# Performance work log

Hardware: AMD Instinct MI355X
Metric: run time of the kernel (lower is better)

The kernel has to match this reference:

```python
import jax, jax.numpy as jnp
import numpy as np

B, M, ND, ED, D, H = 4, 1024, 64, 8, 64, 4
ALPHA = 0.2
NEG = -9.0e15


def setup_inputs() -> dict:
    key = jax.random.key(0)
    ks = jax.random.split(key, 6)
    h = jax.random.normal(ks[0], (B, M, ND), jnp.float32)
    mch_mask = jax.random.randint(ks[1], (B, M, M), 0, 2).astype(jnp.int32)
    comp_val = jax.random.normal(ks[2], (B, M, M, ED), jnp.float32)
    W = jax.random.normal(ks[3], (H, ND, D), jnp.float32) * 0.1
    W_edge = jax.random.normal(ks[4], (H, ED, D), jnp.float32) * 0.1
    a = jax.random.normal(ks[5], (H, 3 * D), jnp.float32) * 0.1
    return {"h": h, "mch_mask": mch_mask, "comp_val": comp_val,
            "W": W, "W_edge": W_edge, "a": a}


def reference(h, mch_mask, comp_val, W, W_edge, a):
    # h: [B,M,ND], mch_mask: [B,M,M], comp_val: [B,M,M,ED]
    # W: [H,ND,D], W_edge: [H,ED,D], a: [H,3D]  (heads stacked)
    d = W.shape[-1]
    a1, a2, a3 = a[:, :d], a[:, d:2 * d], a[:, 2 * d:]
    Wh = jnp.einsum('bmd,hde->bhme', h, W)              # [B,H,M,D]
    Wh1 = jnp.einsum('bhme,he->bhm', Wh, a1)            # [B,H,M]
    Wh2 = jnp.einsum('bhme,he->bhm', Wh, a2)            # [B,H,M]
    # edge_feas = (comp_val @ W_edge) @ a3, fused: comp_val @ (W_edge @ a3)
    w_e = jnp.einsum('hed,hd->he', W_edge, a3)          # [H,ED]
    edge_feas = jnp.einsum('bkqe,he->bhkq', comp_val, w_e)  # [B,H,M,M]
    e = Wh1[:, :, :, None] + Wh2[:, :, None, :] + edge_feas
    e = jnp.where(e > 0, e, ALPHA * e)                  # leaky_relu
    e = jnp.where(mch_mask[:, None, :, :] > 0, e, NEG)
    attn = jax.nn.softmax(e, axis=-1)                   # [B,H,M,M]
    h_prime = jnp.einsum('bhkq,bhqd->bhkd', attn, Wh)   # [B,H,M,D]
    b, nh, m, dd = h_prime.shape
    return h_prime.transpose(0, 2, 1, 3).reshape(b, m, nh * dd)  # concat heads
```

## Files before the change

kernel.cpp:

```cpp
#include <hip/hip_runtime.h>
#include <hip/hip_bf16.h>

#define B_ 4
#define M_ 1024
#define ND_ 64
#define ED_ 8
#define D_ 64
#define H_ 4
#define KT 16
#define QC 64
#define NCH (M_ / QC)
#define ALPHA 0.2f

#define WS_WH1 1048576
#define WS_WH2 1064960
#define WS_WE  1081344

__device__ __forceinline__ float4 f4fma(float s, const float4& v, float4 a) {
    a.x = fmaf(s, v.x, a.x);
    a.y = fmaf(s, v.y, a.y);
    a.z = fmaf(s, v.z, a.z);
    a.w = fmaf(s, v.w, a.w);
    return a;
}

__global__ __launch_bounds__(256) void k_pre(const float* __restrict__ hg,
                                             const float* __restrict__ Wg,
                                             const float* __restrict__ ag,
                                             float* __restrict__ Whg,
                                             float* __restrict__ Wh1g,
                                             float* __restrict__ Wh2g) {
    const int t = threadIdx.x;
    const int g = blockIdx.x * 256 + t;
    const int d = t & 63;
    const int bhm = g >> 6;
    const int m = bhm & (M_ - 1);
    const int h = (bhm >> 10) & (H_ - 1);
    const int b = bhm >> 12;
    const float* hrow = hg + (b * M_ + m) * ND_;
    const float* wcol = Wg + h * ND_ * D_ + d;
    float acc = 0.f;
#pragma unroll
    for (int i = 0; i < ND_; ++i) acc = fmaf(hrow[i], wcol[i * D_], acc);
    Whg[g] = acc;
    float r1 = acc * ag[h * 192 + d];
    float r2 = acc * ag[h * 192 + 64 + d];
#pragma unroll
    for (int off = 32; off >= 1; off >>= 1) {
        r1 += __shfl_xor(r1, off);
        r2 += __shfl_xor(r2, off);
    }
    if (d == 0) {
        Wh1g[(b * H_ + h) * M_ + m] = r1;
        Wh2g[(b * H_ + h) * M_ + m] = r2;
    }
}

__global__ void k_we(const float* __restrict__ Weg, const float* __restrict__ ag,
                     float* __restrict__ weg) {
    const int t = threadIdx.x;
    if (t < H_ * ED_) {
        const int h = t >> 3, e = t & 7;
        const float* wrow = Weg + (h * ED_ + e) * D_;
        const float* a3 = ag + h * 192 + 128;
        float acc = 0.f;
#pragma unroll
        for (int i = 0; i < D_; ++i) acc = fmaf(wrow[i], a3[i], acc);
        weg[t] = acc;
    }
}

__global__ __launch_bounds__(1024) void k_main(const float* __restrict__ cvg,
                                               const int* __restrict__ mg,
                                               const float* __restrict__ Whg,
                                               const float* __restrict__ Wh1g,
                                               const float* __restrict__ Wh2g,
                                               const float* __restrict__ weg,
                                               float* __restrict__ outg) {
    extern __shared__ float smem[];
    float* whl = smem;
    float* pb = smem + 16384;
    float* wel = smem + 20512;
    float* sl = smem + 20544;
    float4* wh4 = (float4*)whl;
    float4* pb4 = (float4*)pb;
    const float4* we4 = (const float4*)wel;

    const int t = threadIdx.x;
    const int lane = t & 63, wv = t >> 6;
    const int b = blockIdx.x >> 6;
    const int k0 = (blockIdx.x & 63) << 4;
    const int hh = lane >> 4, d4 = lane & 15;

    if (t < 32) wel[t] = weg[t];

    const int ek = k0 + wv;
    float wh1r[H_];
#pragma unroll
    for (int h = 0; h < H_; ++h) wh1r[h] = Wh1g[(b * H_ + h) * M_ + ek];

    float4 acc[4];
#pragma unroll
    for (int i = 0; i < 4; ++i) acc[i] = make_float4(0.f, 0.f, 0.f, 0.f);
    float sreg[H_] = {0.f, 0.f, 0.f, 0.f};

    const float4* cvrow = (const float4*)(cvg + (size_t)(b * M_ + ek) * M_ * ED_);
    const int* mrow = mg + (size_t)(b * M_ + ek) * M_;

#pragma unroll
    for (int i = 0; i < 4; ++i) {
        const int ql = wv * 4 + i;
        const float* src = Whg + ((size_t)((b * H_ + hh) * M_) + ql) * D_ + d4 * 4;
        __builtin_amdgcn_global_load_lds((const __attribute__((address_space(1))) void*)src,
                                         (__attribute__((address_space(3))) void*)(whl + ql * 256),
                                         16, 0, 0);
    }
    float4 cv0 = cvrow[lane * 2 + 0];
    float4 cv1 = cvrow[lane * 2 + 1];
    int mk = mrow[lane];
    float wh2r[H_];
#pragma unroll
    for (int h = 0; h < H_; ++h) wh2r[h] = Wh2g[(b * H_ + h) * M_ + lane];

    __syncthreads();

    for (int c = 0; c < NCH; ++c) {
        float pv[H_];
#pragma unroll
        for (int h = 0; h < H_; ++h) {
            const float4 wa = we4[h * 2], wb = we4[h * 2 + 1];
            float ef = cv0.x * wa.x + cv0.y * wa.y + cv0.z * wa.z + cv0.w * wa.w +
                       cv1.x * wb.x + cv1.y * wb.y + cv1.z * wb.z + cv1.w * wb.w;
            float e = wh1r[h] + wh2r[h] + ef;
            e = fmaxf(e, ALPHA * e);
            pv[h] = (mk > 0) ? __expf(e) : 0.0f;
            pb[h * 1032 + wv * QC + lane] = pv[h];
        }
#pragma unroll
        for (int h = 0; h < H_; ++h) {
            float r = pv[h];
#pragma unroll
            for (int off = 32; off >= 1; off >>= 1) r += __shfl_xor(r, off);
            sreg[h] += r;
        }
        __syncthreads();

        if (c + 1 < NCH) {
            const int qn = (c + 1) * QC + lane;
            cv0 = cvrow[qn * 2 + 0];
            cv1 = cvrow[qn * 2 + 1];
            mk = mrow[qn];
#pragma unroll
            for (int h = 0; h < H_; ++h) wh2r[h] = Wh2g[(b * H_ + h) * M_ + qn];
        }

        {
            const int kq = wv >> 2, qg = wv & 3;
#pragma unroll
            for (int j = 0; j < 4; ++j) {
                const int ql = qg * 16 + j * 4;
                const float4 w0 = wh4[(ql + 0) * 64 + lane];
                const float4 w1 = wh4[(ql + 1) * 64 + lane];
                const float4 w2 = wh4[(ql + 2) * 64 + lane];
                const float4 w3 = wh4[(ql + 3) * 64 + lane];
#pragma unroll
                for (int kk = 0; kk < 4; ++kk) {
                    const float4 pq = pb4[hh * 258 + (kq * 4 + kk) * 16 + (ql >> 2)];
                    float4 a = acc[kk];
                    a = f4fma(pq.x, w0, a);
                    a = f4fma(pq.y, w1, a);
                    a = f4fma(pq.z, w2, a);
                    a = f4fma(pq.w, w3, a);
                    acc[kk] = a;
                }
            }
        }
        __syncthreads();

        if (c + 1 < NCH) {
#pragma unroll
            for (int i = 0; i < 4; ++i) {
                const int ql = wv * 4 + i;
                const float* src =
                    Whg + ((size_t)((b * H_ + hh) * M_) + (c + 1) * QC + ql) * D_ + d4 * 4;
                __builtin_amdgcn_global_load_lds(
                    (const __attribute__((address_space(1))) void*)src,
                    (__attribute__((address_space(3))) void*)(whl + ql * 256), 16, 0, 0);
            }
        }
    }

    if (lane == 0) {
#pragma unroll
        for (int h = 0; h < H_; ++h) sl[wv * H_ + h] = sreg[h];
    }
    __syncthreads();
    {
        const int kq = wv >> 2, qg = wv & 3;
#pragma unroll
        for (int kk = 0; kk < 4; ++kk)
            wh4[((kq * 4 + kk) * 4 + qg) * 64 + lane] = acc[kk];
    }
    __syncthreads();
    {
        const float4 r0 = wh4[(wv * 4 + 0) * 64 + lane];
        const float4 r1 = wh4[(wv * 4 + 1) * 64 + lane];
        const float4 r2 = wh4[(wv * 4 + 2) * 64 + lane];
        const float4 r3 = wh4[(wv * 4 + 3) * 64 + lane];
        const float inv = 1.0f / sl[wv * H_ + hh];
        float4 r;
        r.x = (r0.x + r1.x + r2.x + r3.x) * inv;
        r.y = (r0.y + r1.y + r2.y + r3.y) * inv;
        r.z = (r0.z + r1.z + r2.z + r3.z) * inv;
        r.w = (r0.w + r1.w + r2.w + r3.w) * inv;
        float4* o4 = (float4*)(outg + (size_t)(b * M_ + k0 + wv) * (H_ * D_));
        o4[lane] = r;
    }
}

extern "C" void kernel_launch(void* const* d_in, const int* in_sizes, int n_in,
                              void* d_out, int out_size, void* d_ws, size_t ws_size,
                              hipStream_t stream) {
    const float* hg = (const float*)d_in[0];
    const int* mg = (const int*)d_in[1];
    const float* cvg = (const float*)d_in[2];
    const float* Wg = (const float*)d_in[3];
    const float* Weg = (const float*)d_in[4];
    const float* ag = (const float*)d_in[5];
    float* outg = (float*)d_out;
    float* ws = (float*)d_ws;
    float* Whg = ws;
    float* Wh1g = ws + WS_WH1;
    float* Wh2g = ws + WS_WH2;
    float* weg = ws + WS_WE;

    (void)hipFuncSetAttribute((const void*)k_main,
                              hipFuncAttributeMaxDynamicSharedMemorySize, 82432);

    k_pre<<<4096, 256, 0, stream>>>(hg, Wg, ag, Whg, Wh1g, Wh2g);
    k_we<<<1, 64, 0, stream>>>(Weg, ag, weg);
    k_main<<<256, 1024, 82432, stream>>>(cvg, mg, Whg, Wh1g, Wh2g, weg, outg);
}
```

Measured before the change: 274.3 us.

## Restructure attention kernel to 8-row tiles with per-wave q split and tiled projection

The main kernel now processes 8 query rows per 512-thread block instead of 16 per 1024-thread block, doubling the grid. Each wave owns a slice of the key dimension and keeps 8 row accumulators, with a final cross-wave reduction through LDS. Wh staging switches from async global-to-LDS loads to register-staged prefetch with a padded stride to cut bank conflicts, and the softmax row-sum shuffle reduction moves out of the loop. The projection kernel is also rewritten to stage W and h in LDS and compute four outputs per thread. The trade-offs are more register pressure and Wh being reloaded by twice as many blocks.

Measured after the change: 363.1 us. 32.4% more time.

```diff
diff --git a/kernel.cpp b/kernel.cpp
--- a/kernel.cpp
+++ b/kernel.cpp
@@ -1,5 +1,7 @@
 #include <hip/hip_runtime.h>
 #include <hip/hip_bf16.h>
+
+typedef float v4f __attribute__((ext_vector_type(4)));
 
 #define B_ 4
 #define M_ 1024
@@ -7,7 +9,7 @@
 #define ED_ 8
 #define D_ 64
 #define H_ 4
-#define KT 16
+#define KT 8
 #define QC 64
 #define NCH (M_ / QC)
 #define ALPHA 0.2f
@@ -16,12 +18,25 @@
 #define WS_WH2 1064960
 #define WS_WE  1081344
 
-__device__ __forceinline__ float4 f4fma(float s, const float4& v, float4 a) {
-    a.x = fmaf(s, v.x, a.x);
-    a.y = fmaf(s, v.y, a.y);
-    a.z = fmaf(s, v.z, a.z);
-    a.w = fmaf(s, v.w, a.w);
-    return a;
+#define WHL_STRIDE 260
+#define WHL_F (QC * WHL_STRIDE)
+#define PB_H 520
+#define PB_F (H_ * PB_H)
+#define LDS_BYTES ((WHL_F + PB_F + 32 + 32) * 4)
+
+__device__ __forceinline__ v4f splat(float s) { return (v4f){s, s, s, s}; }
+
+__device__ __forceinline__ v4f f4fma(v4f a, v4f b, v4f c) {
+#if __has_builtin(__builtin_elementwise_fma)
+    return __builtin_elementwise_fma(a, b, c);
+#else
+    v4f r;
+    r.x = fmaf(a.x, b.x, c.x);
+    r.y = fmaf(a.y, b.y, c.y);
+    r.z = fmaf(a.z, b.z, c.z);
+    r.w = fmaf(a.w, b.w, c.w);
+    return r;
+#endif
 }
 
 __global__ __launch_bounds__(256) void k_pre(const float* __restrict__ hg,
@@ -30,29 +45,53 @@
                                              float* __restrict__ Whg,
                                              float* __restrict__ Wh1g,
                                              float* __restrict__ Wh2g) {
-    const int t = threadIdx.x;
-    const int g = blockIdx.x * 256 + t;
-    const int d = t & 63;
-    const int bhm = g >> 6;
-    const int m = bhm & (M_ - 1);
-    const int h = (bhm >> 10) & (H_ - 1);
-    const int b = bhm >> 12;
-    const float* hrow = hg + (b * M_ + m) * ND_;
-    const float* wcol = Wg + h * ND_ * D_ + d;
-    float acc = 0.f;
-#pragma unroll
-    for (int i = 0; i < ND_; ++i) acc = fmaf(hrow[i], wcol[i * D_], acc);
-    Whg[g] = acc;
-    float r1 = acc * ag[h * 192 + d];
-    float r2 = acc * ag[h * 192 + 64 + d];
-#pragma unroll
-    for (int off = 32; off >= 1; off >>= 1) {
+    __shared__ float wl[ND_ * D_];
+    __shared__ float hl[16 * 68];
+    const int t = threadIdx.x, lane = t & 63, wv = t >> 6;
+    const int bid = blockIdx.x;
+    const int b = bid >> 8, h = (bid >> 6) & (H_ - 1), mb = bid & 63;
+    const int m0 = mb * 16;
+
+    {
+        const float* wsrc = Wg + h * ND_ * D_;
+#pragma unroll
+        for (int i = 0; i < 4; ++i) {
+            const float* s = wsrc + (wv * 4 + i) * 256 + lane * 4;
+            __builtin_amdgcn_global_load_lds(
+                (const __attribute__((address_space(1))) void*)s,
+                (__attribute__((address_space(3))) void*)(wl + (wv * 4 + i) * 256), 16, 0, 0);
+        }
+    }
+    {
+        const int mh = t >> 4, u = t & 15;
+        v4f hv = *(const v4f*)(hg + ((size_t)(b * M_) + m0 + mh) * ND_ + u * 4);
+        *(v4f*)(hl + mh * 68 + u * 4) = hv;
+    }
+    __syncthreads();
+
+    const int m = t >> 4, d4 = t & 15;
+    v4f acc = {0.f, 0.f, 0.f, 0.f};
+#pragma unroll
+    for (int i = 0; i < ND_; ++i) {
+        v4f w4 = *(const v4f*)(wl + i * 64 + d4 * 4);
+        float hs = hl[m * 68 + i];
+        acc = f4fma(splat(hs), w4, acc);
+    }
+    *(v4f*)(Whg + (((size_t)(b * H_ + h)) * M_ + m0 + m) * D_ + d4 * 4) = acc;
+
+    v4f a1 = *(const v4f*)(ag + h * 192 + d4 * 4);
+    v4f a2 = *(const v4f*)(ag + h * 192 + 64 + d4 * 4);
+    v4f p1 = acc * a1, p2 = acc * a2;
+    float r1 = (p1.x + p1.y) + (p1.z + p1.w);
+    float r2 = (p2.x + p2.y) + (p2.z + p2.w);
+#pragma unroll
+    for (int off = 8; off >= 1; off >>= 1) {
         r1 += __shfl_xor(r1, off);
         r2 += __shfl_xor(r2, off);
     }
-    if (d == 0) {
-        Wh1g[(b * H_ + h) * M_ + m] = r1;
-        Wh2g[(b * H_ + h) * M_ + m] = r2;
+    if (d4 == 0) {
+        Wh1g[((size_t)(b * H_ + h)) * M_ + m0 + m] = r1;
+        Wh2g[((size_t)(b * H_ + h)) * M_ + m0 + m] = r2;
     }
 }
 
@@ -70,26 +109,22 @@
     }
 }
 
-__global__ __launch_bounds__(1024) void k_main(const float* __restrict__ cvg,
-                                               const int* __restrict__ mg,
-                                               const float* __restrict__ Whg,
-                                               const float* __restrict__ Wh1g,
-                                               const float* __restrict__ Wh2g,
-                                               const float* __restrict__ weg,
-                                               float* __restrict__ outg) {
+__global__ __launch_bounds__(512, 4) void k_main(const float* __restrict__ cvg,
+                                                 const int* __restrict__ mg,
+                                                 const float* __restrict__ Whg,
+                                                 const float* __restrict__ Wh1g,
+                                                 const float* __restrict__ Wh2g,
+                                                 const float* __restrict__ weg,
+                                                 float* __restrict__ outg) {
     extern __shared__ float smem[];
     float* whl = smem;
-    float* pb = smem + 16384;
-    float* wel = smem + 20512;
-    float* sl = smem + 20544;
-    float4* wh4 = (float4*)whl;
-    float4* pb4 = (float4*)pb;
-    const float4* we4 = (const float4*)wel;
-
-    const int t = threadIdx.x;
-    const int lane = t & 63, wv = t >> 6;
-    const int b = blockIdx.x >> 6;
-    const int k0 = (blockIdx.x & 63) << 4;
+    float* pb = smem + WHL_F;
+    float* wel = pb + PB_F;
+    float* sl = wel + 32;
+
+    const int t = threadIdx.x, lane = t & 63, wv = t >> 6;
+    const int b = blockIdx.x >> 7;
+    const int k0 = (blockIdx.x & 127) * KT;
     const int hh = lane >> 4, d4 = lane & 15;
 
     if (t < 32) wel[t] = weg[t];
@@ -99,79 +134,79 @@
 #pragma unroll
     for (int h = 0; h < H_; ++h) wh1r[h] = Wh1g[(b * H_ + h) * M_ + ek];
 
-    float4 acc[4];
-#pragma unroll
-    for (int i = 0; i < 4; ++i) acc[i] = make_float4(0.f, 0.f, 0.f, 0.f);
+    const v4f* cvrow = (const v4f*)(cvg + (size_t)(b * M_ + ek) * M_ * ED_);
+    const int* mrow = mg + (size_t)(b * M_ + ek) * M_;
+
+    const int sq = t >> 3, sp = t & 7;
+    const float* wh_src = Whg + ((size_t)(b * H_ + (sp >> 1)) * M_) * D_ + (sp & 1) * 32;
+    float* wh_dst = whl + sq * WHL_STRIDE + sp * 32;
+
+    v4f acc[KT];
+#pragma unroll
+    for (int k = 0; k < KT; ++k) acc[k] = (v4f){0.f, 0.f, 0.f, 0.f};
     float sreg[H_] = {0.f, 0.f, 0.f, 0.f};
 
-    const float4* cvrow = (const float4*)(cvg + (size_t)(b * M_ + ek) * M_ * ED_);
-    const int* mrow = mg + (size_t)(b * M_ + ek) * M_;
-
-#pragma unroll
-    for (int i = 0; i < 4; ++i) {
-        const int ql = wv * 4 + i;
-        const float* src = Whg + ((size_t)((b * H_ + hh) * M_) + ql) * D_ + d4 * 4;
-        __builtin_amdgcn_global_load_lds((const __attribute__((address_space(1))) void*)src,
-                                         (__attribute__((address_space(3))) void*)(whl + ql * 256),
-                                         16, 0, 0);
-    }
-    float4 cv0 = cvrow[lane * 2 + 0];
-    float4 cv1 = cvrow[lane * 2 + 1];
+    v4f cv0 = cvrow[lane * 2], cv1 = cvrow[lane * 2 + 1];
     int mk = mrow[lane];
     float wh2r[H_];
 #pragma unroll
     for (int h = 0; h < H_; ++h) wh2r[h] = Wh2g[(b * H_ + h) * M_ + lane];
-
+    v4f wreg[8];
+    {
+        const v4f* s = (const v4f*)(wh_src + (size_t)sq * D_);
+#pragma unroll
+        for (int i = 0; i < 8; ++i) wreg[i] = s[i];
+#pragma unroll
+        for (int i = 0; i < 8; ++i) ((v4f*)wh_dst)[i] = wreg[i];
+    }
     __syncthreads();
 
     for (int c = 0; c < NCH; ++c) {
-        float pv[H_];
 #pragma unroll
         for (int h = 0; h < H_; ++h) {
-            const float4 wa = we4[h * 2], wb = we4[h * 2 + 1];
-            float ef = cv0.x * wa.x + cv0.y * wa.y + cv0.z * wa.z + cv0.w * wa.w +
-                       cv1.x * wb.x + cv1.y * wb.y + cv1.z * wb.z + cv1.w * wb.w;
+            v4f wa = *(const v4f*)(wel + h * 8);
+            v4f wb = *(const v4f*)(wel + h * 8 + 4);
+            v4f tt = cv0 * wa + cv1 * wb;
+            float ef = (tt.x + tt.y) + (tt.z + tt.w);
             float e = wh1r[h] + wh2r[h] + ef;
             e = fmaxf(e, ALPHA * e);
-            pv[h] = (mk > 0) ? __expf(e) : 0.0f;
-            pb[h * 1032 + wv * QC + lane] = pv[h];
-        }
-#pragma unroll
-        for (int h = 0; h < H_; ++h) {
-            float r = pv[h];
-#pragma unroll
-            for (int off = 32; off >= 1; off >>= 1) r += __shfl_xor(r, off);
-            sreg[h] += r;
+            float p = (mk > 0) ? __expf(e) : 0.0f;
+            pb[h * PB_H + wv * QC + lane] = p;
+            sreg[h] += p;
         }
         __syncthreads();
 
         if (c + 1 < NCH) {
             const int qn = (c + 1) * QC + lane;
-            cv0 = cvrow[qn * 2 + 0];
+            cv0 = cvrow[qn * 2];
             cv1 = cvrow[qn * 2 + 1];
             mk = mrow[qn];
 #pragma unroll
             for (int h = 0; h < H_; ++h) wh2r[h] = Wh2g[(b * H_ + h) * M_ + qn];
+            const v4f* s = (const v4f*)(wh_src + (size_t)((c + 1) * QC + sq) * D_);
+#pragma unroll
+            for (int i = 0; i < 8; ++i) wreg[i] = s[i];
         }
 
         {
-            const int kq = wv >> 2, qg = wv & 3;
-#pragma unroll
-            for (int j = 0; j < 4; ++j) {
-                const int ql = qg * 16 + j * 4;
-                const float4 w0 = wh4[(ql + 0) * 64 + lane];
-                const float4 w1 = wh4[(ql + 1) * 64 + lane];
-                const float4 w2 = wh4[(ql + 2) * 64 + lane];
-                const float4 w3 = wh4[(ql + 3) * 64 + lane];
-#pragma unroll
-                for (int kk = 0; kk < 4; ++kk) {
-                    const float4 pq = pb4[hh * 258 + (kq * 4 + kk) * 16 + (ql >> 2)];
-                    float4 a = acc[kk];
-                    a = f4fma(pq.x, w0, a);
-                    a = f4fma(pq.y, w1, a);
-                    a = f4fma(pq.z, w2, a);
-                    a = f4fma(pq.w, w3, a);
-                    acc[kk] = a;
+            const int q0 = wv * 8;
+#pragma unroll
+            for (int qq = 0; qq < 2; ++qq) {
+                const int q = q0 + qq * 4;
+                const v4f w0 = *(const v4f*)(whl + (q + 0) * WHL_STRIDE + lane * 4);
+                const v4f w1 = *(const v4f*)(whl + (q + 1) * WHL_STRIDE + lane * 4);
+                const v4f w2 = *(const v4f*)(whl + (q + 2) * WHL_STRIDE + lane * 4);
+                const v4f w3 = *(const v4f*)(whl + (q + 3) * WHL_STRIDE + lane * 4);
+                const float* pbase = pb + hh * PB_H + q;
+#pragma unroll
+                for (int k = 0; k < KT; ++k) {
+                    v4f pq = *(const v4f*)(pbase + k * 64);
+                    v4f a = acc[k];
+                    a = f4fma(splat(pq.x), w0, a);
+                    a = f4fma(splat(pq.y), w1, a);
+                    a = f4fma(splat(pq.z), w2, a);
+                    a = f4fma(splat(pq.w), w3, a);
+                    acc[k] = a;
                 }
             }
         }
@@ -179,42 +214,29 @@
 
         if (c + 1 < NCH) {
 #pragma unroll
-            for (int i = 0; i < 4; ++i) {
-                const int ql = wv * 4 + i;
-                const float* src =
-                    Whg + ((size_t)((b * H_ + hh) * M_) + (c + 1) * QC + ql) * D_ + d4 * 4;
-                __builtin_amdgcn_global_load_lds(
-                    (const __attribute__((address_space(1))) void*)src,
-                    (__attribute__((address_space(3))) void*)(whl + ql * 256), 16, 0, 0);
-            }
-        }
-    }
-
-    if (lane == 0) {
-#pragma unroll
-        for (int h = 0; h < H_; ++h) sl[wv * H_ + h] = sreg[h];
-    }
+            for (int i = 0; i < 8; ++i) ((v4f*)wh_dst)[i] = wreg[i];
+        }
+    }
+
+#pragma unroll
+    for (int h = 0; h < H_; ++h) {
+        float r = sreg[h];
+#pragma unroll
+        for (int off = 32; off >= 1; off >>= 1) r += __shfl_xor(r, off);
+        if (lane == 0) sl[wv * H_ + h] = r;
+    }
+#pragma unroll
+    for (int k = 0; k < KT; ++k)
+        *(v4f*)(whl + (wv * KT + k) * WHL_STRIDE + lane * 4) = acc[k];
     __syncthreads();
     {
-        const int kq = wv >> 2, qg = wv & 3;
-#pragma unroll
-        for (int kk = 0; kk < 4; ++kk)
-            wh4[((kq * 4 + kk) * 4 + qg) * 64 + lane] = acc[kk];
-    }
-    __syncthreads();
-    {
-        const float4 r0 = wh4[(wv * 4 + 0) * 64 + lane];
-        const float4 r1 = wh4[(wv * 4 + 1) * 64 + lane];
-        const float4 r2 = wh4[(wv * 4 + 2) * 64 + lane];
-        const float4 r3 = wh4[(wv * 4 + 3) * 64 + lane];
+        v4f r = (v4f){0.f, 0.f, 0.f, 0.f};
+#pragma unroll
+        for (int p = 0; p < 8; ++p)
+            r += *(const v4f*)(whl + (p * KT + wv) * WHL_STRIDE + lane * 4);
         const float inv = 1.0f / sl[wv * H_ + hh];
-        float4 r;
-        r.x = (r0.x + r1.x + r2.x + r3.x) * inv;
-        r.y = (r0.y + r1.y + r2.y + r3.y) * inv;
-        r.z = (r0.z + r1.z + r2.z + r3.z) * inv;
-        r.w = (r0.w + r1.w + r2.w + r3.w) * inv;
-        float4* o4 = (float4*)(outg + (size_t)(b * M_ + k0 + wv) * (H_ * D_));
-        o4[lane] = r;
+        r *= splat(inv);
+        *(v4f*)(outg + (size_t)(b * M_ + k0 + wv) * (H_ * D_) + lane * 4) = r;
     }
 }
 
@@ -235,9 +257,9 @@
     float* weg = ws + WS_WE;
 
     (void)hipFuncSetAttribute((const void*)k_main,
-                              hipFuncAttributeMaxDynamicSharedMemorySize, 82432);
-
-    k_pre<<<4096, 256, 0, stream>>>(hg, Wg, ag, Whg, Wh1g, Wh2g);
+                              hipFuncAttributeMaxDynamicSharedMemorySize, LDS_BYTES);
+
+    k_pre<<<1024, 256, 0, stream>>>(hg, Wg, ag, Whg, Wh1g, Wh2g);
     k_we<<<1, 64, 0, stream>>>(Weg, ag, weg);
-    k_main<<<256, 1024, 82432, stream>>>(cvg, mg, Whg, Wh1g, Wh2g, weg, outg);
-}
+    k_main<<<512, 512, LDS_BYTES, stream>>>(cvg, mg, Whg, Wh1g, Wh2g, weg, outg);
+}
```
